# Kernel tuning notes

Measured on AMD Instinct MI355X. Metric: run time of the kernel, lower is better.

The kernel has to match this reference:

```python
import jax, jax.numpy as jnp
import numpy as np

IMAGE_SIZE = 256
PSIZE = 6
STRIDE = 2
WINDOW = IMAGE_SIZE + 1 - PSIZE  # 251
CUR = np.arange(0, WINDOW, STRIDE)
if CUR[-1] != WINDOW - 1:
    CUR = np.concatenate([CUR, np.array([WINDOW - 1])])
NPOS = len(CUR)  # 126 strided window positions per axis
BATCH = 128


def setup_inputs() -> dict:
    key = jax.random.key(0)
    x = jax.random.normal(key, (BATCH, 1, IMAGE_SIZE, IMAGE_SIZE), dtype=jnp.float32)
    return {"x": x}


def reference(x):
    # Equivalent to patch_tf.forward(to_patch): for each strided window position
    # (r, c) in CUR x CUR and each in-patch offset (i, j) in [0, PSIZE)^2,
    # output[b, r*NPOS + c, i*PSIZE + j] = x[b, 0, r + i, c + j].
    cur = jnp.asarray(CUR, dtype=jnp.int32)          # [NPOS]
    off = jnp.arange(PSIZE, dtype=jnp.int32)         # [PSIZE]
    row_idx = cur[:, None] + off[None, :]            # [NPOS, PSIZE]
    col_idx = cur[:, None] + off[None, :]            # [NPOS, PSIZE]
    img = x[:, 0]                                    # [B, H, W]
    # Advanced-index gather -> [B, NPOS, NPOS, PSIZE, PSIZE]
    patches = img[:, row_idx[:, None, :, None], col_idx[None, :, None, :]]
    return patches.reshape(x.shape[0], NPOS * NPOS, PSIZE * PSIZE)
```

## Files before the change

### kernel.cpp

```cpp
#include <hip/hip_runtime.h>


#define IMG 256
#define PSZ 6
#define NPOS 126
#define BATCHN 128
#define LDSW 267
#define NXCD 8

typedef float f32x4 __attribute__((ext_vector_type(4)));

__global__ __launch_bounds__(256) void image2patch_kernel(
    const float* __restrict__ x, float* __restrict__ out) {
  __shared__ float tile[PSZ * LDSW];

  const int cpx = (BATCHN * NPOS) / NXCD;
  const int raw = blockIdx.x;
  const int blk = (raw % NXCD) * cpx + raw / NXCD;

  const int b = blk / NPOS;
  const int i = blk - b * NPOS;
  const int t = threadIdx.x;

  const float* src = x + (size_t)b * (IMG * IMG) + (size_t)(2 * i) * IMG;
  for (int idx = t; idx < PSZ * (IMG / 4); idx += 256) {
    const int col4 = idx / PSZ;
    const int row  = idx - col4 * PSZ;
    float4 v = reinterpret_cast<const float4*>(src + row * IMG)[col4];
    float* d = &tile[row * LDSW + col4 * 4];
    d[0] = v.x; d[1] = v.y; d[2] = v.z; d[3] = v.w;
  }
  __syncthreads();

  if (t < 252) {
    const int tj = t / 9;
    const int m  = t - 9 * tj;
    const int k0 = 4 * m;
    const int kA = k0,     rA = kA / PSZ, cA = 2 * tj + (kA - PSZ * rA);
    const int kB = k0 + 1, rB = kB / PSZ, cB = 2 * tj + (kB - PSZ * rB);
    const int kC = k0 + 2, rC = kC / PSZ, cC = 2 * tj + (kC - PSZ * rC);
    const int kD = k0 + 3, rD = kD / PSZ, cD = 2 * tj + (kD - PSZ * rD);
    const int a0 = rA * LDSW + cA;
    const int a1 = rB * LDSW + cB;
    const int a2 = rC * LDSW + cC;
    const int a3 = rD * LDSW + cD;

    f32x4 g0, g1, g2, g3, g4;
    g0.x = tile[a0      ]; g0.y = tile[a1      ]; g0.z = tile[a2      ]; g0.w = tile[a3      ];
    g1.x = tile[a0 +  56]; g1.y = tile[a1 +  56]; g1.z = tile[a2 +  56]; g1.w = tile[a3 +  56];
    g2.x = tile[a0 + 112]; g2.y = tile[a1 + 112]; g2.z = tile[a2 + 112]; g2.w = tile[a3 + 112];
    g3.x = tile[a0 + 168]; g3.y = tile[a1 + 168]; g3.z = tile[a2 + 168]; g3.w = tile[a3 + 168];
    if (t < 126) {
      g4.x = tile[a0 + 224]; g4.y = tile[a1 + 224]; g4.z = tile[a2 + 224]; g4.w = tile[a3 + 224];
    }

    f32x4* outp = reinterpret_cast<f32x4*>(
        out + ((size_t)b * (NPOS * NPOS) + (size_t)i * NPOS) * (PSZ * PSZ));
    __builtin_nontemporal_store(g0, outp + t);
    __builtin_nontemporal_store(g1, outp + t + 252);
    __builtin_nontemporal_store(g2, outp + t + 504);
    __builtin_nontemporal_store(g3, outp + t + 756);
    if (t < 126) {
      __builtin_nontemporal_store(g4, outp + t + 1008);
    }
  }
}

extern "C" void kernel_launch(void* const* d_in, const int* in_sizes, int n_in,
                              void* d_out, int out_size, void* d_ws, size_t ws_size,
                              hipStream_t stream) {
  const float* x = (const float*)d_in[0];
  float* out = (float*)d_out;
  image2patch_kernel<<<BATCHN * NPOS, 256, 0, stream>>>(x, out);
}
```

Before: 317.3 us.

## Process two window rows per 512-thread block sharing an eight-row LDS tile

Each block now handles two consecutive patch-row positions, loading eight image rows into LDS once instead of six rows per position. The overlapping rows are reused between the two bands, and the loop-based global load becomes a single float4 load per thread. This cuts redundant global reads and halves the block count, at the cost of larger blocks and shared memory per block.

```diff
diff --git a/kernel.cpp b/kernel.cpp
--- a/kernel.cpp
+++ b/kernel.cpp
@@ -6,62 +6,69 @@
 #define NPOS 126
 #define BATCHN 128
 #define LDSW 267
+#define IPB 2
+#define NIB (NPOS / IPB)
+#define NBLK (BATCHN * NIB)
 #define NXCD 8
 
 typedef float f32x4 __attribute__((ext_vector_type(4)));
 
-__global__ __launch_bounds__(256) void image2patch_kernel(
+__global__ __launch_bounds__(512) void image2patch_kernel(
     const float* __restrict__ x, float* __restrict__ out) {
-  __shared__ float tile[PSZ * LDSW];
+  __shared__ float tile[8 * LDSW];
 
-  const int cpx = (BATCHN * NPOS) / NXCD;
+  const int cpx = NBLK / NXCD;
   const int raw = blockIdx.x;
   const int blk = (raw % NXCD) * cpx + raw / NXCD;
 
-  const int b = blk / NPOS;
-  const int i = blk - b * NPOS;
-  const int t = threadIdx.x;
+  const int b  = blk / NIB;
+  const int i0 = (blk - b * NIB) * IPB;
+  const int t  = threadIdx.x;
 
-  const float* src = x + (size_t)b * (IMG * IMG) + (size_t)(2 * i) * IMG;
-  for (int idx = t; idx < PSZ * (IMG / 4); idx += 256) {
-    const int col4 = idx / PSZ;
-    const int row  = idx - col4 * PSZ;
-    float4 v = reinterpret_cast<const float4*>(src + row * IMG)[col4];
+  {
+    const int row  = t & 7;
+    const int col4 = t >> 3;
+    const float* src = x + (size_t)b * (IMG * IMG) + (size_t)(2 * i0 + row) * IMG;
+    float4 v = reinterpret_cast<const float4*>(src)[col4];
     float* d = &tile[row * LDSW + col4 * 4];
     d[0] = v.x; d[1] = v.y; d[2] = v.z; d[3] = v.w;
   }
   __syncthreads();
 
-  if (t < 252) {
-    const int tj = t / 9;
-    const int m  = t - 9 * tj;
+  const int band = t >> 8;
+  const int tl   = t & 255;
+  if (tl < 252) {
+    const int tj = tl / 9;
+    const int m  = tl - 9 * tj;
     const int k0 = 4 * m;
     const int kA = k0,     rA = kA / PSZ, cA = 2 * tj + (kA - PSZ * rA);
     const int kB = k0 + 1, rB = kB / PSZ, cB = 2 * tj + (kB - PSZ * rB);
     const int kC = k0 + 2, rC = kC / PSZ, cC = 2 * tj + (kC - PSZ * rC);
     const int kD = k0 + 3, rD = kD / PSZ, cD = 2 * tj + (kD - PSZ * rD);
-    const int a0 = rA * LDSW + cA;
-    const int a1 = rB * LDSW + cB;
-    const int a2 = rC * LDSW + cC;
-    const int a3 = rD * LDSW + cD;
+    const int base = 2 * band * LDSW;
+    const int a0 = base + rA * LDSW + cA;
+    const int a1 = base + rB * LDSW + cB;
+    const int a2 = base + rC * LDSW + cC;
+    const int a3 = base + rD * LDSW + cD;
 
     f32x4 g0, g1, g2, g3, g4;
     g0.x = tile[a0      ]; g0.y = tile[a1      ]; g0.z = tile[a2      ]; g0.w = tile[a3      ];
     g1.x = tile[a0 +  56]; g1.y = tile[a1 +  56]; g1.z = tile[a2 +  56]; g1.w = tile[a3 +  56];
     g2.x = tile[a0 + 112]; g2.y = tile[a1 + 112]; g2.z = tile[a2 + 112]; g2.w = tile[a3 + 112];
     g3.x = tile[a0 + 168]; g3.y = tile[a1 + 168]; g3.z = tile[a2 + 168]; g3.w = tile[a3 + 168];
-    if (t < 126) {
+    if (tl < 126) {
       g4.x = tile[a0 + 224]; g4.y = tile[a1 + 224]; g4.z = tile[a2 + 224]; g4.w = tile[a3 + 224];
     }
 
+    const int i = i0 + band;
     f32x4* outp = reinterpret_cast<f32x4*>(
         out + ((size_t)b * (NPOS * NPOS) + (size_t)i * NPOS) * (PSZ * PSZ));
-    __builtin_nontemporal_store(g0, outp + t);
-    __builtin_nontemporal_store(g1, outp + t + 252);
-    __builtin_nontemporal_store(g2, outp + t + 504);
-    __builtin_nontemporal_store(g3, outp + t + 756);
-    if (t < 126) {
-      __builtin_nontemporal_store(g4, outp + t + 1008);
+    __builtin_nontemporal_store(g0, outp + tl);
+    __builtin_nontemporal_store(g1, outp + tl + 252);
+    __builtin_nontemporal_store(g2, outp + tl + 504);
+    __builtin_nontemporal_store(g3, outp + tl + 756);
+    if (tl < 126) {
+      __builtin_nontemporal_store(g4, outp + tl + 1008);
     }
   }
 }
@@ -71,5 +78,5 @@
                               hipStream_t stream) {
   const float* x = (const float*)d_in[0];
   float* out = (float*)d_out;
-  image2patch_kernel<<<BATCHN * NPOS, 256, 0, stream>>>(x, out);
+  image2patch_kernel<<<NBLK, 512, 0, stream>>>(x, out);
 }
```

Result: no change. 318.6 us (+0.4%).
